# Optimization experiments

Hardware: AMD Instinct MI355X
Metric: run time of the kernel (lower is better)

Reference implementation:

```python
import jax, jax.numpy as jnp
import numpy as np

K, D = 4096, 256
BETA, DECAY, EPS = 0.25, 0.99, 1e-05
B = 32768


def setup_inputs() -> dict:
    key = jax.random.key(0)
    k1, k2, k3, k4 = jax.random.split(key, 4)
    return {
        "z_e": jax.random.normal(k1, (B, D), dtype=jnp.float32),
        "codebook": jax.random.normal(k2, (K, D), dtype=jnp.float32),
        "ema_cluster_size": jax.random.uniform(k3, (K,), dtype=jnp.float32),
        "ema_weight": jax.random.normal(k4, (K, D), dtype=jnp.float32),
    }


def reference(z_e, codebook, ema_cluster_size, ema_weight):
    z_e = z_e.astype(jnp.float32)
    # squared L2 distances: ||z||^2 - 2 z.C^T + ||C||^2  (chunking in torch is
    # purely a memory optimization; math is identical)
    e_norm = jnp.sum(z_e * z_e, axis=1, keepdims=True)            # [B,1]
    c_norm = jnp.sum(codebook * codebook, axis=1)                  # [K]
    dists = e_norm - 2.0 * (z_e @ codebook.T) + c_norm[None, :]    # [B,K]
    idx = jnp.argmin(dists, axis=1)                                # [B] int

    z_q = codebook[idx]                                            # [B,d] gather

    # EMA codebook update (no_grad in torch)
    counts = jnp.zeros((K,), jnp.float32).at[idx].add(1.0)         # bincount
    new_cluster = ema_cluster_size * DECAY + counts * (1.0 - DECAY)
    dw = jnp.zeros((K, D), jnp.float32).at[idx].add(z_e)           # index_add_
    new_ema_weight = ema_weight * DECAY + dw * (1.0 - DECAY)
    n = jnp.sum(new_cluster)
    cluster_size = (new_cluster + EPS) / (n + K * EPS) * n
    new_codebook = new_ema_weight / cluster_size[:, None]

    z_q_ste = z_e + jax.lax.stop_gradient(z_q - z_e)
    commit = BETA * jnp.mean((z_e - z_q) ** 2)
    return (z_q_ste, idx, commit, new_codebook, new_cluster, new_ema_weight)
```

## Files before the change

### kernel.cpp

```cpp
#include <hip/hip_runtime.h>

#define KC 4096
#define DD 256
#define BB 32768
#define P_BETA 0.25f
#define P_DECAY 0.99f
#define P_EPS 1e-5f
#define TAU 0.5f
#define CHUNK 16

typedef __attribute__((ext_vector_type(8))) short bf16x8;
typedef __attribute__((ext_vector_type(4))) float f32x4;

static __device__ __forceinline__ unsigned short f2bf(float f) {
    unsigned int u = __float_as_uint(f);
    unsigned int r = (u + 0x7fffu + ((u >> 16) & 1u)) >> 16;
    return (unsigned short)r;
}
static __device__ __forceinline__ void gload_lds16(const void* g, void* s) {
    __builtin_amdgcn_global_load_lds(
        (const __attribute__((address_space(1))) unsigned int*)g,
        (__attribute__((address_space(3))) unsigned int*)s, 16, 0, 0);
}

#define ZBLK (BB * DD / 4 / 256)
#define CBLK (KC * DD / 4 / 256)
#define EBLK (KC * DD / 4 / 256)
__global__ __launch_bounds__(256) void convert_all_kernel(
    const float* __restrict__ z, const float* __restrict__ cb,
    unsigned short* __restrict__ zb, unsigned short* __restrict__ cbb,
    float* __restrict__ cn, int* __restrict__ cnt,
    const float* __restrict__ ema_w, float* __restrict__ out_emaw) {
    const int b = blockIdx.x;
    if (b < ZBLK) {
        int t = b * 256 + threadIdx.x;
        float4 v = ((const float4*)z)[t];
        *(ushort4*)&zb[(size_t)t * 4] =
            make_ushort4(f2bf(v.x), f2bf(v.y), f2bf(v.z), f2bf(v.w));
    } else if (b < ZBLK + CBLK) {
        int t = (b - ZBLK) * 256 + threadIdx.x;
        int lane = threadIdx.x & 63;
        int row = (b - ZBLK) * 4 + (threadIdx.x >> 6);
        float4 v = ((const float4*)cb)[t];
        *(ushort4*)&cbb[(size_t)t * 4] =
            make_ushort4(f2bf(v.x), f2bf(v.y), f2bf(v.z), f2bf(v.w));
        float s = v.x * v.x + v.y * v.y + v.z * v.z + v.w * v.w;
#pragma unroll
        for (int m = 32; m; m >>= 1) s += __shfl_xor(s, m);
        if (lane == 0) cn[row] = s;
    } else if (b == ZBLK + CBLK) {
        int4* p = (int4*)cnt;
        int4 zv = make_int4(0, 0, 0, 0);
#pragma unroll
        for (int j = 0; j < 4; ++j) p[threadIdx.x * 4 + j] = zv;
    } else {
        int t = (b - ZBLK - CBLK - 1) * 256 + threadIdx.x;
        float4 v = ((const float4*)ema_w)[t];
        ((float4*)out_emaw)[t] =
            make_float4(v.x * P_DECAY, v.y * P_DECAY, v.z * P_DECAY, v.w * P_DECAY);
    }
}

__global__ __launch_bounds__(256, 2) void
mfma_argmin_kernel(const unsigned short* __restrict__ zb,
                   const unsigned short* __restrict__ cbb,
                   const float* __restrict__ cn,
                   float4* __restrict__ cand) {
    __shared__ unsigned short As[128 * 256];
    __shared__ unsigned short Bs[128 * 64];

    const int tid = threadIdx.x;
    const int l = tid & 63, w = tid >> 6;
    const int xcd = blockIdx.x & 7;
    const int half = xcd >> 2;
    const int rb = (blockIdx.x >> 3) * 4 + (xcd & 3);
    const int row0 = rb * 128;
    const int col0 = half * 2048;
    const int wm = w & 1, wn = w >> 1;
    const int m_off = wm * 64, n_off = wn * 64;
    const int lm = l & 15, lq = l >> 4;

    {
        const int lrow = w * 2 + (l >> 5);
        const int coff = ((l & 31) ^ lrow) * 8;
#pragma unroll
        for (int i = 0; i < 16; ++i) {
            gload_lds16(zb + (size_t)(row0 + i * 8 + lrow) * DD + coff,
                        &As[(i * 8 + w * 2) * 256]);
        }
    }

    const int srow = l >> 3;
    const int scol = ((l & 7) ^ srow) * 8;
    const int g0 = w * 4;

    float best[16];
    int bidx[16];
#pragma unroll
    for (int s = 0; s < 16; ++s) { best[s] = 3.4e38f; bidx[s] = 0; }

    for (int kc = 0; kc < 2048; kc += 128) {
        f32x4 acc[4][4];
#pragma unroll
        for (int a = 0; a < 4; ++a)
#pragma unroll
            for (int b = 0; b < 4; ++b) acc[a][b] = (f32x4){0.f, 0.f, 0.f, 0.f};

        for (int dc = 0; dc < 4; ++dc) {
#pragma unroll
            for (int j = 0; j < 4; ++j) {
                const int g = g0 + j;
                const int br = col0 + kc + g * 8 + srow;
                gload_lds16(cbb + (size_t)br * DD + dc * 64 + scol, &Bs[g * 512]);
            }
            __syncthreads();
#pragma unroll
            for (int ks = 0; ks < 2; ++ks) {
                bf16x8 af[4], bfr[4];
                const int cbi = dc * 8 + ks * 4 + lq;
#pragma unroll
                for (int tm = 0; tm < 4; ++tm) {
                    int r = m_off + tm * 16 + lm;
                    af[tm] = *(const bf16x8*)&As[r * 256 + ((cbi ^ (r & 7)) * 8)];
                }
#pragma unroll
                for (int tn = 0; tn < 4; ++tn) {
                    int r = n_off + tn * 16 + lm;
                    bfr[tn] = *(const bf16x8*)&Bs[r * 64 + (((ks * 4 + lq) ^ (r & 7)) * 8)];
                }
#pragma unroll
                for (int tm = 0; tm < 4; ++tm)
#pragma unroll
                    for (int tn = 0; tn < 4; ++tn)
                        acc[tm][tn] = __builtin_amdgcn_mfma_f32_16x16x32_bf16(
                            af[tm], bfr[tn], acc[tm][tn], 0, 0, 0);
            }
            __syncthreads();
        }
#pragma unroll
        for (int tn = 0; tn < 4; ++tn) {
            const int col = col0 + kc + n_off + tn * 16 + lm;
            const float cnv = cn[col];
#pragma unroll
            for (int tm = 0; tm < 4; ++tm)
#pragma unroll
                for (int r = 0; r < 4; ++r) {
                    float dist = fmaf(-2.0f, acc[tm][tn][r], cnv);
                    int s = tm * 4 + r;
                    if (dist < best[s]) { best[s] = dist; bidx[s] = col; }
                }
        }
    }

    float v2[16];
    int i2[16];
#pragma unroll
    for (int s = 0; s < 16; ++s) { v2[s] = 3.4e38f; i2[s] = 0x7fffffff; }
#pragma unroll
    for (int m = 1; m < 16; m <<= 1) {
#pragma unroll
        for (int s = 0; s < 16; ++s) {
            float w1 = __shfl_xor(best[s], m); int j1 = __shfl_xor(bidx[s], m);
            float w2 = __shfl_xor(v2[s], m);   int j2 = __shfl_xor(i2[s], m);
            bool b = (w1 < best[s]) || (w1 == best[s] && j1 < bidx[s]);
            if (b) {
                bool c = (best[s] < w2) || (best[s] == w2 && bidx[s] < j2);
                v2[s] = c ? best[s] : w2; i2[s] = c ? bidx[s] : j2;
                best[s] = w1; bidx[s] = j1;
            } else {
                bool c = (w1 < v2[s]) || (w1 == v2[s] && j1 < i2[s]);
                v2[s] = c ? w1 : v2[s]; i2[s] = c ? j1 : i2[s];
            }
        }
    }

    float4* red = (float4*)As;
    if (lm == 0) {
#pragma unroll
        for (int tm = 0; tm < 4; ++tm)
#pragma unroll
            for (int r = 0; r < 4; ++r) {
                int s = tm * 4 + r;
                int row_local = m_off + tm * 16 + lq * 4 + r;
                red[wn * 128 + row_local] =
                    make_float4(best[s], __int_as_float(bidx[s]), v2[s], __int_as_float(i2[s]));
            }
    }
    __syncthreads();
    if (tid < 128) {
        float4 a = red[tid], b = red[128 + tid];
        float av1 = a.x, av2 = a.z; int ai1 = __float_as_int(a.y), ai2 = __float_as_int(a.w);
        float bv1 = b.x, bv2 = b.z; int bi1 = __float_as_int(b.y), bi2 = __float_as_int(b.w);
        float v1o, v2o; int i1o, i2o;
        bool bb = (bv1 < av1) || (bv1 == av1 && bi1 < ai1);
        if (bb) {
            v1o = bv1; i1o = bi1;
            bool c = (av1 < bv2) || (av1 == bv2 && ai1 < bi2);
            v2o = c ? av1 : bv2; i2o = c ? ai1 : bi2;
        } else {
            v1o = av1; i1o = ai1;
            bool c = (bv1 < av2) || (bv1 == av2 && bi1 < ai2);
            v2o = c ? bv1 : av2; i2o = c ? bi1 : ai2;
        }
        cand[(size_t)half * BB + row0 + tid] =
            make_float4(v1o, __int_as_float(i1o), v2o, __int_as_float(i2o));
    }
}

__global__ __launch_bounds__(256) void merge_zq_kernel(
    const float4* __restrict__ cand, const float* __restrict__ z,
    const float* __restrict__ cb, const float* __restrict__ cn,
    int* __restrict__ idx_i, float* __restrict__ idx_f,
    int* __restrict__ cnt, float* __restrict__ zq,
    float* __restrict__ commit_parts) {
    const int w = threadIdx.x >> 6, l = threadIdx.x & 63;
    const int i = blockIdx.x * 4 + w;
    float4 a = cand[i], b = cand[(size_t)BB + i];
    float av1 = a.x, av2 = a.z; int ai1 = __float_as_int(a.y), ai2 = __float_as_int(a.w);
    float bv1 = b.x, bv2 = b.z; int bi1 = __float_as_int(b.y), bi2 = __float_as_int(b.w);
    float v1o, v2o; int i1o, i2o;
    bool bb = (bv1 < av1) || (bv1 == av1 && bi1 < ai1);
    if (bb) {
        v1o = bv1; i1o = bi1;
        bool c = (av1 < bv2) || (av1 == bv2 && ai1 < bi2);
        v2o = c ? av1 : bv2; i2o = c ? ai1 : bi2;
    } else {
        v1o = av1; i1o = ai1;
        bool c = (bv1 < av2) || (bv1 == av2 && bi1 < ai2);
        v2o = c ? bv1 : av2; i2o = c ? bi1 : ai2;
    }
    float4 zv = ((const float4*)z)[(size_t)i * 64 + l];
    float4 p = ((const float4*)cb)[(size_t)i1o * 64 + l];
    int kb = i1o;
    float4 cv = p;
    if (v2o - v1o < TAU) {
        float4 q = ((const float4*)cb)[(size_t)i2o * 64 + l];
        float s1 = zv.x * p.x + zv.y * p.y + zv.z * p.z + zv.w * p.w;
        float s2 = zv.x * q.x + zv.y * q.y + zv.z * q.z + zv.w * q.w;
#pragma unroll
        for (int m = 32; m; m >>= 1) {
            s1 += __shfl_xor(s1, m);
            s2 += __shfl_xor(s2, m);
        }
        float d1 = cn[i1o] - 2.f * s1;
        float d2 = cn[i2o] - 2.f * s2;
        if (d2 < d1 || (d2 == d1 && i2o < i1o)) { kb = i2o; cv = q; }
    }
    ((float4*)zq)[(size_t)i * 64 + l] = cv;
    float dx = zv.x - cv.x, dy = zv.y - cv.y, dz = zv.z - cv.z, dq = zv.w - cv.w;
    float s = dx * dx + dy * dy + dz * dz + dq * dq;
#pragma unroll
    for (int m = 32; m; m >>= 1) s += __shfl_xor(s, m);
    __shared__ float ls[4];
    if (l == 0) {
        ls[w] = s;
        idx_i[i] = kb;
        idx_f[i] = (float)kb;
        atomicAdd(&cnt[kb], 1);
    }
    __syncthreads();
    if (threadIdx.x == 0) commit_parts[blockIdx.x] = ls[0] + ls[1] + ls[2] + ls[3];
}

__global__ __launch_bounds__(256) void prefix_kernel(
    const int* __restrict__ cnt, int* __restrict__ cursor,
    const float* __restrict__ ema_cs, float* __restrict__ out_cluster,
    float* __restrict__ n_ws) {
    __shared__ int ls[257];
    __shared__ float lns[4];
    const int t = threadIdx.x;
    int local[16];
    int s = 0;
    float ns = 0.f;
#pragma unroll
    for (int j = 0; j < 16; ++j) {
        int c = cnt[t * 16 + j];
        local[j] = s; s += c;
        float nc = ema_cs[t * 16 + j] * P_DECAY + (float)c * (1.0f - P_DECAY);
        out_cluster[t * 16 + j] = nc;
        ns += nc;
    }
    ls[t + 1] = s;
#pragma unroll
    for (int m = 32; m; m >>= 1) ns += __shfl_xor(ns, m);
    if ((t & 63) == 0) lns[t >> 6] = ns;
    __syncthreads();
    if (t == 0) {
        ls[0] = 0;
        for (int j = 1; j <= 256; ++j) ls[j] += ls[j - 1];
        *n_ws = lns[0] + lns[1] + lns[2] + lns[3];
    }
    __syncthreads();
    int off = ls[t];
#pragma unroll
    for (int j = 0; j < 16; ++j) cursor[t * 16 + j] = off + local[j];
}

__global__ __launch_bounds__(256) void scatter_kernel(
    const int* __restrict__ idx_i, int* __restrict__ cursor,
    int* __restrict__ row_of) {
    const int i = blockIdx.x * 256 + threadIdx.x;
    const int k = idx_i[i];
    int pos = atomicAdd(&cursor[k], 1);
    row_of[pos] = i | (k << 16);
}

__global__ __launch_bounds__(256) void bucket_scatter_kernel(
    const float* __restrict__ z, const int* __restrict__ row_of,
    float* __restrict__ out_emaw, const float* __restrict__ commit_parts,
    float* __restrict__ out_commit) {
    const int t = threadIdx.x;
    if (blockIdx.x == BB / CHUNK) {
        float cs = 0.f;
        for (int j = t; j < BB / 4; j += 256) cs += commit_parts[j];
#pragma unroll
        for (int m = 32; m; m >>= 1) cs += __shfl_xor(cs, m);
        __shared__ float lc[4];
        if ((t & 63) == 0) lc[t >> 6] = cs;
        __syncthreads();
        if (t == 0)
            *out_commit = P_BETA * (lc[0] + lc[1] + lc[2] + lc[3]) / (float)((size_t)BB * DD);
        return;
    }
    __shared__ int pk[CHUNK];
    const int p0 = blockIdx.x * CHUNK;
    if (t < CHUNK) pk[t] = row_of[p0 + t];
    __syncthreads();
    float acc = 0.f;
    int kprev = pk[0] >> 16;
#pragma unroll 4
    for (int j = 0; j < CHUNK; ++j) {
        int p = pk[j];
        int r = p & 0xffff, k = p >> 16;
        if (k != kprev) {
            atomicAdd(&out_emaw[(size_t)kprev * DD + t], acc * (1.0f - P_DECAY));
            acc = 0.f;
            kprev = k;
        }
        acc += z[(size_t)r * DD + t];
    }
    atomicAdd(&out_emaw[(size_t)kprev * DD + t], acc * (1.0f - P_DECAY));
}

__global__ __launch_bounds__(256) void codebook_kernel(
    const float* __restrict__ out_emaw, const float* __restrict__ out_cluster,
    const float* __restrict__ n_ws, float* __restrict__ out_codebook) {
    const int id4 = blockIdx.x * 256 + threadIdx.x;
    const int k = id4 >> 6;
    const float n = *n_ws;
    float4 v = ((const float4*)out_emaw)[id4];
    float cl = out_cluster[k];
    float inv = 1.0f / ((cl + P_EPS) / (n + (float)KC * P_EPS) * n);
    ((float4*)out_codebook)[id4] =
        make_float4(v.x * inv, v.y * inv, v.z * inv, v.w * inv);
}

extern "C" void kernel_launch(void* const* d_in, const int* in_sizes, int n_in,
                              void* d_out, int out_size, void* d_ws, size_t ws_size,
                              hipStream_t stream) {
    const float* z      = (const float*)d_in[0];
    const float* cb     = (const float*)d_in[1];
    const float* ema_cs = (const float*)d_in[2];
    const float* ema_w  = (const float*)d_in[3];

    float4* cand = (float4*)d_ws;
    unsigned short* zb = (unsigned short*)(cand + 2 * (size_t)BB);
    unsigned short* cbb = zb + (size_t)BB * DD;
    float* c_norm = (float*)(cbb + (size_t)KC * DD);
    int* idx_i = (int*)(c_norm + KC);
    int* cnt = idx_i + BB;
    int* cursor = cnt + KC;
    int* row_of = cursor + KC;
    float* commit_parts = (float*)(row_of + BB);
    float* n_ws = commit_parts + BB / 4;

    float* out        = (float*)d_out;
    float* o_zq       = out;
    float* o_idx      = o_zq + (size_t)BB * DD;
    float* o_commit   = o_idx + BB;
    float* o_codebook = o_commit + 1;
    float* o_cluster  = o_codebook + (size_t)KC * DD;
    float* o_emaw     = o_cluster + KC;

    convert_all_kernel<<<ZBLK + CBLK + 1 + EBLK, 256, 0, stream>>>(
        z, cb, zb, cbb, c_norm, cnt, ema_w, o_emaw);
    mfma_argmin_kernel<<<(BB / 128) * 2, 256, 0, stream>>>(zb, cbb, c_norm, cand);
    merge_zq_kernel<<<BB / 4, 256, 0, stream>>>(cand, z, cb, c_norm, idx_i,
                                                o_idx, cnt, o_zq, commit_parts);
    prefix_kernel<<<1, 256, 0, stream>>>(cnt, cursor, ema_cs, o_cluster, n_ws);
    scatter_kernel<<<BB / 256, 256, 0, stream>>>(idx_i, cursor, row_of);
    bucket_scatter_kernel<<<BB / CHUNK + 1, 256, 0, stream>>>(
        z, row_of, o_emaw, commit_parts, o_commit);
    codebook_kernel<<<(KC * DD / 4) / 256, 256, 0, stream>>>(
        o_emaw, o_cluster, n_ws, o_codebook);
    (void)in_sizes; (void)n_in; (void)out_size; (void)ws_size;
}
```

Measured before the change: 226.9 us.

## Read bf16 z copy in merge and EMA scatter; fuse prefix with scatter

The merge kernel now loads fp32 z only for rows whose top-2 candidates are close, and computes the commitment loss from the bf16 copy. The EMA weight accumulation also sums bf16 z, which halves the bytes read on those paths. The prefix and row-scatter kernels are merged into one single-block kernel that uses LDS cursors, removing a launch. In exchange, the commitment loss and EMA weights lose precision, and the scatter now runs serially on one workgroup.

```diff
diff --git a/kernel.cpp b/kernel.cpp
--- a/kernel.cpp
+++ b/kernel.cpp
@@ -16,6 +16,9 @@
     unsigned int u = __float_as_uint(f);
     unsigned int r = (u + 0x7fffu + ((u >> 16) & 1u)) >> 16;
     return (unsigned short)r;
+}
+static __device__ __forceinline__ float b2f(unsigned short u) {
+    return __uint_as_float((unsigned int)u << 16);
 }
 static __device__ __forceinline__ void gload_lds16(const void* g, void* s) {
     __builtin_amdgcn_global_load_lds(
@@ -209,6 +212,7 @@
 
 __global__ __launch_bounds__(256) void merge_zq_kernel(
     const float4* __restrict__ cand, const float* __restrict__ z,
+    const unsigned short* __restrict__ zb,
     const float* __restrict__ cb, const float* __restrict__ cn,
     int* __restrict__ idx_i, float* __restrict__ idx_f,
     int* __restrict__ cnt, float* __restrict__ zq,
@@ -229,11 +233,11 @@
         bool c = (bv1 < av2) || (bv1 == av2 && bi1 < ai2);
         v2o = c ? bv1 : av2; i2o = c ? bi1 : ai2;
     }
-    float4 zv = ((const float4*)z)[(size_t)i * 64 + l];
     float4 p = ((const float4*)cb)[(size_t)i1o * 64 + l];
     int kb = i1o;
     float4 cv = p;
     if (v2o - v1o < TAU) {
+        float4 zv = ((const float4*)z)[(size_t)i * 64 + l];
         float4 q = ((const float4*)cb)[(size_t)i2o * 64 + l];
         float s1 = zv.x * p.x + zv.y * p.y + zv.z * p.z + zv.w * p.w;
         float s2 = zv.x * q.x + zv.y * q.y + zv.z * q.z + zv.w * q.w;
@@ -247,7 +251,9 @@
         if (d2 < d1 || (d2 == d1 && i2o < i1o)) { kb = i2o; cv = q; }
     }
     ((float4*)zq)[(size_t)i * 64 + l] = cv;
-    float dx = zv.x - cv.x, dy = zv.y - cv.y, dz = zv.z - cv.z, dq = zv.w - cv.w;
+    ushort4 zu = *(const ushort4*)&zb[(size_t)i * DD + l * 4];
+    float dx = b2f(zu.x) - cv.x, dy = b2f(zu.y) - cv.y;
+    float dz = b2f(zu.z) - cv.z, dq = b2f(zu.w) - cv.w;
     float s = dx * dx + dy * dy + dz * dz + dq * dq;
 #pragma unroll
     for (int m = 32; m; m >>= 1) s += __shfl_xor(s, m);
@@ -262,12 +268,13 @@
     if (threadIdx.x == 0) commit_parts[blockIdx.x] = ls[0] + ls[1] + ls[2] + ls[3];
 }
 
-__global__ __launch_bounds__(256) void prefix_kernel(
-    const int* __restrict__ cnt, int* __restrict__ cursor,
+__global__ __launch_bounds__(256) void prefix_scatter_kernel(
+    const int* __restrict__ cnt, const int* __restrict__ idx_i,
     const float* __restrict__ ema_cs, float* __restrict__ out_cluster,
-    float* __restrict__ n_ws) {
+    float* __restrict__ n_ws, int* __restrict__ row_of) {
     __shared__ int ls[257];
     __shared__ float lns[4];
+    __shared__ int cur[KC];
     const int t = threadIdx.x;
     int local[16];
     int s = 0;
@@ -293,20 +300,18 @@
     __syncthreads();
     int off = ls[t];
 #pragma unroll
-    for (int j = 0; j < 16; ++j) cursor[t * 16 + j] = off + local[j];
-}
-
-__global__ __launch_bounds__(256) void scatter_kernel(
-    const int* __restrict__ idx_i, int* __restrict__ cursor,
-    int* __restrict__ row_of) {
-    const int i = blockIdx.x * 256 + threadIdx.x;
-    const int k = idx_i[i];
-    int pos = atomicAdd(&cursor[k], 1);
-    row_of[pos] = i | (k << 16);
+    for (int j = 0; j < 16; ++j) cur[t * 16 + j] = off + local[j];
+    __syncthreads();
+    for (int j = 0; j < BB / 256; ++j) {
+        int i = j * 256 + t;
+        int k = idx_i[i];
+        int pos = atomicAdd(&cur[k], 1);
+        row_of[pos] = i | (k << 16);
+    }
 }
 
 __global__ __launch_bounds__(256) void bucket_scatter_kernel(
-    const float* __restrict__ z, const int* __restrict__ row_of,
+    const unsigned short* __restrict__ zb, const int* __restrict__ row_of,
     float* __restrict__ out_emaw, const float* __restrict__ commit_parts,
     float* __restrict__ out_commit) {
     const int t = threadIdx.x;
@@ -337,7 +342,7 @@
             acc = 0.f;
             kprev = k;
         }
-        acc += z[(size_t)r * DD + t];
+        acc += b2f(zb[(size_t)r * DD + t]);
     }
     atomicAdd(&out_emaw[(size_t)kprev * DD + t], acc * (1.0f - P_DECAY));
 }
@@ -369,8 +374,7 @@
     float* c_norm = (float*)(cbb + (size_t)KC * DD);
     int* idx_i = (int*)(c_norm + KC);
     int* cnt = idx_i + BB;
-    int* cursor = cnt + KC;
-    int* row_of = cursor + KC;
+    int* row_of = cnt + KC;
     float* commit_parts = (float*)(row_of + BB);
     float* n_ws = commit_parts + BB / 4;
 
@@ -385,12 +389,12 @@
     convert_all_kernel<<<ZBLK + CBLK + 1 + EBLK, 256, 0, stream>>>(
         z, cb, zb, cbb, c_norm, cnt, ema_w, o_emaw);
     mfma_argmin_kernel<<<(BB / 128) * 2, 256, 0, stream>>>(zb, cbb, c_norm, cand);
-    merge_zq_kernel<<<BB / 4, 256, 0, stream>>>(cand, z, cb, c_norm, idx_i,
+    merge_zq_kernel<<<BB / 4, 256, 0, stream>>>(cand, z, zb, cb, c_norm, idx_i,
                                                 o_idx, cnt, o_zq, commit_parts);
-    prefix_kernel<<<1, 256, 0, stream>>>(cnt, cursor, ema_cs, o_cluster, n_ws);
-    scatter_kernel<<<BB / 256, 256, 0, stream>>>(idx_i, cursor, row_of);
+    prefix_scatter_kernel<<<1, 256, 0, stream>>>(cnt, idx_i, ema_cs, o_cluster,
+                                                 n_ws, row_of);
     bucket_scatter_kernel<<<BB / CHUNK + 1, 256, 0, stream>>>(
-        z, row_of, o_emaw, commit_parts, o_commit);
+        zb, row_of, o_emaw, commit_parts, o_commit);
     codebook_kernel<<<(KC * DD / 4) / 256, 256, 0, stream>>>(
         o_emaw, o_cluster, n_ws, o_codebook);
     (void)in_sizes; (void)n_in; (void)out_size; (void)ws_size;
```

Result: slower. 249.7 us (+10.1%).

## Double-buffer codebook tiles in LDS to overlap global loads with MFMA

Applied to the files above, without the earlier changes.

Splits the codebook LDS tile into two half-width buffers (32 d-columns each) and prefetches the next stage while the current one feeds MFMAs. The old code waited on a barrier after each load and again after compute. The new loop has one barrier per stage over 128 smaller stages. The goal is to hide global-to-LDS latency. The cost is more frequent barriers and a different swizzle pattern.

```diff
diff --git a/kernel.cpp b/kernel.cpp
--- a/kernel.cpp
+++ b/kernel.cpp
@@ -67,7 +67,7 @@
                    const float* __restrict__ cn,
                    float4* __restrict__ cand) {
     __shared__ unsigned short As[128 * 256];
-    __shared__ unsigned short Bs[128 * 64];
+    __shared__ unsigned short Bs[2][128 * 32];
 
     const int tid = threadIdx.x;
     const int l = tid & 63, w = tid >> 6;
@@ -90,53 +90,63 @@
         }
     }
 
-    const int srow = l >> 3;
-    const int scol = ((l & 7) ^ srow) * 8;
-    const int g0 = w * 4;
+    const int srow2 = l >> 2;
+    const int scol2 = ((l & 3) ^ (srow2 & 3)) * 8;
+    const int g0b = w * 2;
+    auto stageB = [&](int buf, int ns) {
+        const int kcn = (ns >> 3) * 128;
+        const int dcn = (ns & 7) * 32;
+#pragma unroll
+        for (int j = 0; j < 2; ++j) {
+            const int g = g0b + j;
+            const int br = col0 + kcn + g * 16 + srow2;
+            gload_lds16(cbb + (size_t)br * DD + dcn + scol2, &Bs[buf][g * 512]);
+        }
+    };
+
+    stageB(0, 0);
+    __syncthreads();
 
     float best[16];
     int bidx[16];
 #pragma unroll
     for (int s = 0; s < 16; ++s) { best[s] = 3.4e38f; bidx[s] = 0; }
 
-    for (int kc = 0; kc < 2048; kc += 128) {
+    int cur = 0;
+    for (int kci = 0; kci < 16; ++kci) {
         f32x4 acc[4][4];
 #pragma unroll
         for (int a = 0; a < 4; ++a)
 #pragma unroll
             for (int b = 0; b < 4; ++b) acc[a][b] = (f32x4){0.f, 0.f, 0.f, 0.f};
 
-        for (int dc = 0; dc < 4; ++dc) {
-#pragma unroll
-            for (int j = 0; j < 4; ++j) {
-                const int g = g0 + j;
-                const int br = col0 + kc + g * 8 + srow;
-                gload_lds16(cbb + (size_t)br * DD + dc * 64 + scol, &Bs[g * 512]);
+#pragma unroll
+        for (int st = 0; st < 8; ++st) {
+            const int ns = kci * 8 + st + 1;
+            if (ns < 128) stageB(cur ^ 1, ns);
+            bf16x8 af[4], bfr[4];
+            const int cbi = st * 4 + lq;
+#pragma unroll
+            for (int tn = 0; tn < 4; ++tn) {
+                int r = n_off + tn * 16 + lm;
+                bfr[tn] = *(const bf16x8*)&Bs[cur][r * 32 + ((lq ^ (r & 3)) * 8)];
             }
+#pragma unroll
+            for (int tm = 0; tm < 4; ++tm) {
+                int r = m_off + tm * 16 + lm;
+                af[tm] = *(const bf16x8*)&As[r * 256 + ((cbi ^ (r & 7)) * 8)];
+            }
+#pragma unroll
+            for (int tm = 0; tm < 4; ++tm)
+#pragma unroll
+                for (int tn = 0; tn < 4; ++tn)
+                    acc[tm][tn] = __builtin_amdgcn_mfma_f32_16x16x32_bf16(
+                        af[tm], bfr[tn], acc[tm][tn], 0, 0, 0);
             __syncthreads();
-#pragma unroll
-            for (int ks = 0; ks < 2; ++ks) {
-                bf16x8 af[4], bfr[4];
-                const int cbi = dc * 8 + ks * 4 + lq;
-#pragma unroll
-                for (int tm = 0; tm < 4; ++tm) {
-                    int r = m_off + tm * 16 + lm;
-                    af[tm] = *(const bf16x8*)&As[r * 256 + ((cbi ^ (r & 7)) * 8)];
-                }
-#pragma unroll
-                for (int tn = 0; tn < 4; ++tn) {
-                    int r = n_off + tn * 16 + lm;
-                    bfr[tn] = *(const bf16x8*)&Bs[r * 64 + (((ks * 4 + lq) ^ (r & 7)) * 8)];
-                }
-#pragma unroll
-                for (int tm = 0; tm < 4; ++tm)
-#pragma unroll
-                    for (int tn = 0; tn < 4; ++tn)
-                        acc[tm][tn] = __builtin_amdgcn_mfma_f32_16x16x32_bf16(
-                            af[tm], bfr[tn], acc[tm][tn], 0, 0, 0);
-            }
-            __syncthreads();
-        }
+            cur ^= 1;
+        }
+
+        const int kc = kci * 128;
 #pragma unroll
         for (int tn = 0; tn < 4; ++tn) {
             const int col = col0 + kc + n_off + tn * 16 + lm;
```

Result: slower. 234.0 us (+3.1%).
